# Kernel tuning notes

Hardware: AMD Instinct MI355X
Metric: run time of the kernel (lower is better)

## Reference

```python
import jax, jax.numpy as jnp
import numpy as np

D_MODEL = 512
D_STATE = 16
D_CONV = 4
EXPAND = 2
D_INNER = EXPAND * D_MODEL          # 1024
DT_RANK = D_MODEL // 16             # 32 (canonical 'auto' dt_rank)
EPS = 1e-5


def setup_inputs() -> dict:
    key = jax.random.key(0)
    ks = jax.random.split(key, 12)
    w = lambda i, shape, s=0.02: (jax.random.normal(ks[i], shape, jnp.float32) * s)
    inp = {
        "x": jax.random.normal(ks[0], (2, 1024, D_MODEL), jnp.float32),
        # pre-mixer LayerNorm
        "ln1_g": jnp.ones((D_MODEL,), jnp.float32),
        "ln1_b": jnp.zeros((D_MODEL,), jnp.float32),
        # Mamba SSM params
        "in_proj_w": w(1, (2 * D_INNER, D_MODEL)),
        "conv_w": w(2, (D_INNER, D_CONV), 0.1),
        "conv_b": jnp.zeros((D_INNER,), jnp.float32),
        "x_proj_w": w(3, (DT_RANK + 2 * D_STATE, D_INNER)),
        "dt_proj_w": w(4, (D_INNER, DT_RANK), 0.1),
        "dt_proj_b": w(5, (D_INNER,), 0.1),
        "A_log": jnp.log(jnp.broadcast_to(
            jnp.arange(1, D_STATE + 1, dtype=jnp.float32), (D_INNER, D_STATE))),
        "D": jnp.ones((D_INNER,), jnp.float32),
        "out_proj_w": w(6, (D_MODEL, D_INNER)),
        # FFN sub-block
        "ln2_g": jnp.ones((D_MODEL,), jnp.float32),
        "ln2_b": jnp.zeros((D_MODEL,), jnp.float32),
        "ffn1_w": w(7, (4 * D_MODEL, D_MODEL)),
        "ffn1_b": jnp.zeros((4 * D_MODEL,), jnp.float32),
        "ffn2_w": w(8, (D_MODEL, 4 * D_MODEL)),
        "ffn2_b": jnp.zeros((D_MODEL,), jnp.float32),
    }
    return inp


def _layernorm(x, g, b):
    mu = jnp.mean(x, axis=-1, keepdims=True)
    var = jnp.var(x, axis=-1, keepdims=True)
    return (x - mu) * jax.lax.rsqrt(var + EPS) * g + b


def _mamba(x, in_proj_w, conv_w, conv_b, x_proj_w, dt_proj_w, dt_proj_b,
           A_log, D, out_proj_w):
    B, L, _ = x.shape
    # input projection -> (x_in, gate z), each [B, L, E]
    xz = jnp.einsum('bld,ed->ble', x, in_proj_w)
    xi, z = jnp.split(xz, 2, axis=-1)
    # depthwise causal conv1d (width D_CONV): left-pad, cross-correlate
    xp = jnp.pad(xi, ((0, 0), (D_CONV - 1, 0), (0, 0)))
    xc = conv_b
    for k in range(D_CONV):
        xc = xc + xp[:, k:k + L, :] * conv_w[:, k]
    xc = jax.nn.silu(xc)  # [B, L, E]
    # data-dependent SSM parameters
    x_dbl = jnp.einsum('ble,re->blr', xc, x_proj_w)
    dt, Bc, Cc = jnp.split(x_dbl, [DT_RANK, DT_RANK + D_STATE], axis=-1)
    delta = jax.nn.softplus(jnp.einsum('blr,er->ble', dt, dt_proj_w) + dt_proj_b)
    A = -jnp.exp(A_log)  # [E, N]
    # discretize: deltaA, deltaBx both [B, L, E, N]
    deltaA = jnp.exp(delta[..., None] * A)
    deltaBx = delta[..., None] * Bc[:, :, None, :] * xc[..., None]

    def step(h, inputs):
        dA, dBx, C = inputs                       # [B,E,N],[B,E,N],[B,N]
        h = dA * h + dBx
        y = jnp.einsum('ben,bn->be', h, C)
        return h, y

    h0 = jnp.zeros((B, D_INNER, D_STATE), x.dtype)
    _, ys = jax.lax.scan(step, h0,
                         (jnp.swapaxes(deltaA, 0, 1),
                          jnp.swapaxes(deltaBx, 0, 1),
                          jnp.swapaxes(Cc, 0, 1)))
    y = jnp.swapaxes(ys, 0, 1) + xc * D           # [B, L, E]
    y = y * jax.nn.silu(z)
    return jnp.einsum('ble,de->bld', y, out_proj_w)


def reference(x, ln1_g, ln1_b, in_proj_w, conv_w, conv_b, x_proj_w,
              dt_proj_w, dt_proj_b, A_log, D, out_proj_w,
              ln2_g, ln2_b, ffn1_w, ffn1_b, ffn2_w, ffn2_b):
    # pre-norm Mamba mixer + residual (dropout = identity in eval mode)
    h = _mamba(_layernorm(x, ln1_g, ln1_b), in_proj_w, conv_w, conv_b,
               x_proj_w, dt_proj_w, dt_proj_b, A_log, D, out_proj_w)
    x = x + h
    # pre-norm FFN + residual
    f = _layernorm(x, ln2_g, ln2_b)
    f = jax.nn.gelu(jnp.einsum('bld,fd->blf', f, ffn1_w) + ffn1_b)
    f = jnp.einsum('blf,df->bld', f, ffn2_w) + ffn2_b
    return x + f
```

## Files before the change

kernel.cpp:

```cpp
#include <hip/hip_runtime.h>
#include <cmath>

typedef unsigned short u16;
typedef __attribute__((ext_vector_type(8))) short bf16x8;
typedef __attribute__((ext_vector_type(4))) float f32x4;

#define BB    2
#define LSEQ  1024
#define DM    512
#define DI    1024
#define NTOK  2048
#define NC    64
#define CL    16

__device__ __forceinline__ float siluf(float x) {
    return x * (1.0f / (1.0f + __expf(-x)));
}
__device__ __forceinline__ float geluf(float x) {
    float c = 0.7978845608028654f * (x + 0.044715f * x * x * x);
    return 0.5f * x * (1.0f + tanhf(c));
}
__device__ __forceinline__ u16 f2bf(float f) {
    union { float f; unsigned u; } v; v.f = f;
    unsigned r = v.u + 0x7fff + ((v.u >> 16) & 1);
    return (u16)(r >> 16);
}
__device__ __forceinline__ float bf2f(u16 u) {
    union { unsigned u; float f; } v; v.u = ((unsigned)u) << 16; return v.f;
}
__device__ __forceinline__ void async_cp16(const u16* g, u16* l) {
    __builtin_amdgcn_global_load_lds(
        (const __attribute__((address_space(1))) void*)g,
        (__attribute__((address_space(3))) void*)l, 16, 0, 0);
}

#define NCVT 3680

__global__ void prep_kernel(const float* __restrict__ s0, u16* __restrict__ d0,
                            const float* __restrict__ s1, u16* __restrict__ d1,
                            const float* __restrict__ s2, u16* __restrict__ d2,
                            const float* __restrict__ s3, u16* __restrict__ d3,
                            const float* __restrict__ s4, u16* __restrict__ d4,
                            const float* __restrict__ s5, u16* __restrict__ d5,
                            const float* __restrict__ x, const float* __restrict__ g,
                            const float* __restrict__ b, u16* __restrict__ lnb)
{
    __shared__ float shs[4], shq[4];
    __shared__ float smu, srs;
    if (blockIdx.x < NCVT) {
        int i = (blockIdx.x * 256 + threadIdx.x) * 4;
        const float* sp; u16* dp; int off;
        if      (i < 1048576) { sp = s0; dp = d0; off = i; }
        else if (i < 1572864) { sp = s1; dp = d1; off = i - 1048576; }
        else if (i < 2621440) { sp = s2; dp = d2; off = i - 1572864; }
        else if (i < 3670016) { sp = s3; dp = d3; off = i - 2621440; }
        else if (i < 3735552) { sp = s4; dp = d4; off = i - 3670016; }
        else                  { sp = s5; dp = d5; off = i - 3735552; }
        float4 v = *(const float4*)(sp + off);
        ushort4 o;
        o.x = f2bf(v.x); o.y = f2bf(v.y); o.z = f2bf(v.z); o.w = f2bf(v.w);
        *(ushort4*)(dp + off) = o;
        return;
    }
    int t = blockIdx.x - NCVT;
    int tid = threadIdx.x;
    const float* xr = x + (size_t)t * DM;
    float v0 = xr[tid];
    float v1 = xr[tid + 256];
    float rsum = v0 + v1;
    float rsq  = v0 * v0 + v1 * v1;
    #pragma unroll
    for (int o = 32; o > 0; o >>= 1) { rsum += __shfl_down(rsum, o); rsq += __shfl_down(rsq, o); }
    int wid = tid >> 6, lane = tid & 63;
    if (lane == 0) { shs[wid] = rsum; shq[wid] = rsq; }
    __syncthreads();
    if (tid == 0) {
        float a  = shs[0] + shs[1] + shs[2] + shs[3];
        float a2 = shq[0] + shq[1] + shq[2] + shq[3];
        float mu = a / DM;
        float var = a2 / DM - mu * mu;
        smu = mu;
        srs = rsqrtf(var + 1e-5f);
    }
    __syncthreads();
    float mu = smu, rs = srs;
    u16* orow = lnb + (size_t)t * DM;
    orow[tid]       = f2bf((v0 - mu) * rs * g[tid]       + b[tid]);
    orow[tid + 256] = f2bf((v1 - mu) * rs * g[tid + 256] + b[tid + 256]);
}

__global__ void ln_bf16_kernel(const float* __restrict__ x, const float* __restrict__ g,
                               const float* __restrict__ b, u16* __restrict__ out)
{
    int t = blockIdx.x;
    int tid = threadIdx.x;
    const float* xr = x + (size_t)t * DM;
    float v0 = xr[tid];
    float v1 = xr[tid + 256];
    float rsum = v0 + v1;
    float rsq  = v0 * v0 + v1 * v1;
    #pragma unroll
    for (int o = 32; o > 0; o >>= 1) { rsum += __shfl_down(rsum, o); rsq += __shfl_down(rsq, o); }
    __shared__ float shs[4], shq[4];
    __shared__ float smu, srs;
    int wid = tid >> 6, lane = tid & 63;
    if (lane == 0) { shs[wid] = rsum; shq[wid] = rsq; }
    __syncthreads();
    if (tid == 0) {
        float a  = shs[0] + shs[1] + shs[2] + shs[3];
        float a2 = shq[0] + shq[1] + shq[2] + shq[3];
        float mu = a / DM;
        float var = a2 / DM - mu * mu;
        smu = mu;
        srs = rsqrtf(var + 1e-5f);
    }
    __syncthreads();
    float mu = smu, rs = srs;
    u16* orow = out + (size_t)t * DM;
    orow[tid]       = f2bf((v0 - mu) * rs * g[tid]       + b[tid]);
    orow[tid + 256] = f2bf((v1 - mu) * rs * g[tid + 256] + b[tid + 256]);
}

template<int EPI, int BM, int BN, int BK, int OBF>
__global__ __launch_bounds__(256)
void mgemm_kernel(const u16* __restrict__ A, const u16* __restrict__ W, int K,
                  void* __restrict__ Cp, int ldc,
                  const float* __restrict__ bias, const float* __restrict__ resid, int ldr)
{
    __shared__ u16 As[BM * BK];
    __shared__ u16 Bs[BN * BK];
    constexpr int WR = BM / 2, WC = BN / 2;
    constexpr int MR = WR / 16, NR = WC / 16;
    constexpr int LPR = BK / 8;
    constexpr int CH_ROWS = 64 / LPR;
    constexpr int NCH_A = BM / CH_ROWS, NCH_B = BN / CH_ROWS;

    const int tid = threadIdx.x;
    const int wave = tid >> 6, lane = tid & 63;
    const int wm = wave >> 1, wn = wave & 1;
    const int m0 = blockIdx.y * BM, n0 = blockIdx.x * BN;
    const int crow = lane / LPR, ckoff = (lane % LPR) * 8;
    const int fr = lane & 15;

    f32x4 acc[MR][NR] = {};

    for (int k0 = 0; k0 < K; k0 += BK) {
        for (int c = wave; c < NCH_A; c += 4)
            async_cp16(A + (size_t)(m0 + c * CH_ROWS + crow) * K + k0 + ckoff, &As[c * 512]);
        for (int c = wave; c < NCH_B; c += 4)
            async_cp16(W + (size_t)(n0 + c * CH_ROWS + crow) * K + k0 + ckoff, &Bs[c * 512]);
        __syncthreads();
        #pragma unroll
        for (int ks = 0; ks < BK / 32; ++ks) {
            const int fk = ks * 32 + ((lane >> 4) << 3);
            bf16x8 af[MR], bv[NR];
            #pragma unroll
            for (int i = 0; i < MR; ++i)
                af[i] = *(const bf16x8*)&As[(wm * WR + i * 16 + fr) * BK + fk];
            #pragma unroll
            for (int j = 0; j < NR; ++j)
                bv[j] = *(const bf16x8*)&Bs[(wn * WC + j * 16 + fr) * BK + fk];
            #pragma unroll
            for (int i = 0; i < MR; ++i)
                #pragma unroll
                for (int j = 0; j < NR; ++j)
                    acc[i][j] = __builtin_amdgcn_mfma_f32_16x16x32_bf16(af[i], bv[j], acc[i][j], 0, 0, 0);
        }
        __syncthreads();
    }

    const int rbase = (lane >> 4) << 2;
    #pragma unroll
    for (int i = 0; i < MR; ++i) {
        #pragma unroll
        for (int j = 0; j < NR; ++j) {
            const int col  = n0 + wn * WC + j * 16 + fr;
            const int row0 = m0 + wm * WR + i * 16 + rbase;
            float bvv = (EPI == 4) ? bias[col] : 0.0f;
            #pragma unroll
            for (int r = 0; r < 4; ++r) {
                float v = acc[i][j][r];
                if (EPI == 3) v += resid[(size_t)(row0 + r) * ldr + col];
                if (EPI == 4) v += bvv + resid[(size_t)(row0 + r) * ldr + col];
                if (OBF) ((u16*)Cp)[(size_t)(row0 + r) * ldc + col] = f2bf(v);
                else     ((float*)Cp)[(size_t)(row0 + r) * ldc + col] = v;
            }
        }
    }
}

template<int EPI, int OBF>
__global__ __launch_bounds__(512)
void mgemm8_kernel(const u16* __restrict__ A, const u16* __restrict__ W, int K,
                   void* __restrict__ Cp, int ldc, const float* __restrict__ bias)
{
    constexpr int BM = 128, BN = 128, BK = 64;
    __shared__ u16 As[BM * BK];
    __shared__ u16 Bs[BN * BK];
    const int tid = threadIdx.x;
    const int wave = tid >> 6, lane = tid & 63;
    const int wm = wave >> 2, wn = wave & 3;
    const int m0 = blockIdx.y * BM, n0 = blockIdx.x * BN;
    const int crow = lane >> 3, ckoff = (lane & 7) * 8;
    const int fr = lane & 15;

    f32x4 acc[4][2] = {};

    for (int k0 = 0; k0 < K; k0 += BK) {
        #pragma unroll
        for (int c = wave; c < 16; c += 8)
            async_cp16(A + (size_t)(m0 + c * 8 + crow) * K + k0 + ckoff, &As[c * 512]);
        #pragma unroll
        for (int c = wave; c < 16; c += 8)
            async_cp16(W + (size_t)(n0 + c * 8 + crow) * K + k0 + ckoff, &Bs[c * 512]);
        __syncthreads();
        #pragma unroll
        for (int ks = 0; ks < 2; ++ks) {
            const int fk = ks * 32 + ((lane >> 4) << 3);
            bf16x8 af[4], bv[2];
            #pragma unroll
            for (int i = 0; i < 4; ++i)
                af[i] = *(const bf16x8*)&As[(wm * 64 + i * 16 + fr) * BK + fk];
            #pragma unroll
            for (int j = 0; j < 2; ++j)
                bv[j] = *(const bf16x8*)&Bs[(wn * 32 + j * 16 + fr) * BK + fk];
            #pragma unroll
            for (int i = 0; i < 4; ++i)
                #pragma unroll
                for (int j = 0; j < 2; ++j)
                    acc[i][j] = __builtin_amdgcn_mfma_f32_16x16x32_bf16(af[i], bv[j], acc[i][j], 0, 0, 0);
        }
        __syncthreads();
    }

    const int rbase = (lane >> 4) << 2;
    #pragma unroll
    for (int i = 0; i < 4; ++i) {
        #pragma unroll
        for (int j = 0; j < 2; ++j) {
            const int col  = n0 + wn * 32 + j * 16 + fr;
            const int row0 = m0 + wm * 64 + i * 16 + rbase;
            float bvv = (EPI == 2) ? bias[col] : 0.0f;
            #pragma unroll
            for (int r = 0; r < 4; ++r) {
                float v = acc[i][j][r];
                if (EPI == 2) v = geluf(v + bvv);
                if (OBF) ((u16*)Cp)[(size_t)(row0 + r) * ldc + col] = f2bf(v);
                else     ((float*)Cp)[(size_t)(row0 + r) * ldc + col] = v;
            }
        }
    }
}

__global__ __launch_bounds__(256)
void xproj_part_kernel(const u16* __restrict__ A, const u16* __restrict__ W,
                       float* __restrict__ P)
{
    constexpr int BM = 64, BK = 128;
    __shared__ u16 As[BM * BK];
    __shared__ u16 Bs[64 * BK];
    const int tid = threadIdx.x;
    const int wave = tid >> 6, lane = tid & 63;
    const int wm = wave >> 1, wn = wave & 1;
    const int ks = blockIdx.x;
    const int m0 = blockIdx.y * BM;
    const int k0 = ks * BK;
    const int crow = lane >> 4, ckoff = (lane & 15) * 8;
    const int fr = lane & 15;

    for (int c = wave; c < 16; c += 4) {
        async_cp16(A + (size_t)(m0 + c * 4 + crow) * 1024 + k0 + ckoff, &As[c * 512]);
        async_cp16(W + (size_t)(c * 4 + crow) * 1024 + k0 + ckoff, &Bs[c * 512]);
    }
    __syncthreads();

    f32x4 acc[2][2] = {};
    #pragma unroll
    for (int ks2 = 0; ks2 < 4; ++ks2) {
        const int fk = ks2 * 32 + ((lane >> 4) << 3);
        bf16x8 af[2], bv[2];
        #pragma unroll
        for (int i = 0; i < 2; ++i)
            af[i] = *(const bf16x8*)&As[(wm * 32 + i * 16 + fr) * BK + fk];
        #pragma unroll
        for (int j = 0; j < 2; ++j)
            bv[j] = *(const bf16x8*)&Bs[(wn * 32 + j * 16 + fr) * BK + fk];
        #pragma unroll
        for (int i = 0; i < 2; ++i)
            #pragma unroll
            for (int j = 0; j < 2; ++j)
                acc[i][j] = __builtin_amdgcn_mfma_f32_16x16x32_bf16(af[i], bv[j], acc[i][j], 0, 0, 0);
    }

    const int rbase = (lane >> 4) << 2;
    float* Pk = P + (size_t)ks * NTOK * 64;
    #pragma unroll
    for (int i = 0; i < 2; ++i)
        #pragma unroll
        for (int j = 0; j < 2; ++j) {
            const int col  = wn * 32 + j * 16 + fr;
            const int row0 = m0 + wm * 32 + i * 16 + rbase;
            #pragma unroll
            for (int r = 0; r < 4; ++r)
                Pk[(size_t)(row0 + r) * 64 + col] = acc[i][j][r];
        }
}

__global__ void xproj_reduce_kernel(const float* __restrict__ P, float* __restrict__ xdbl,
                                    u16* __restrict__ dtb)
{
    int i = blockIdx.x * 256 + threadIdx.x;
    float s = 0.0f;
    #pragma unroll
    for (int ks = 0; ks < 8; ++ks) s += P[(size_t)ks * NTOK * 64 + i];
    xdbl[i] = s;
    int col = i & 63;
    if (col < 32) dtb[(i >> 6) * 32 + col] = f2bf(s);
}

__global__ void conv_silu_kernel(const u16* __restrict__ xz,
                                 const float* __restrict__ cw,
                                 const float* __restrict__ cb,
                                 u16* __restrict__ xcb)
{
    int idx = blockIdx.x * 256 + threadIdx.x;
    int e8 = idx & (DI / 8 - 1);
    int e  = e8 * 8;
    int t  = idx >> 7;
    int l  = t & (LSEQ - 1);
    const u16* base = xz + (size_t)t * 2048 + e;
    bf16x8 r0 = {}, r1 = {}, r2 = {}, r3;
    r3 = *(const bf16x8*)(base);
    if (l >= 1) r2 = *(const bf16x8*)(base - 2048);
    if (l >= 2) r1 = *(const bf16x8*)(base - 2 * 2048);
    if (l >= 3) r0 = *(const bf16x8*)(base - 3 * 2048);
    float o[8];
    #pragma unroll
    for (int j = 0; j < 8; ++j) {
        const float4 w = *(const float4*)(cw + (e + j) * 4);
        float acc = cb[e + j];
        acc = fmaf(bf2f((u16)r0[j]), w.x, acc);
        acc = fmaf(bf2f((u16)r1[j]), w.y, acc);
        acc = fmaf(bf2f((u16)r2[j]), w.z, acc);
        acc = fmaf(bf2f((u16)r3[j]), w.w, acc);
        o[j] = siluf(acc);
    }
    bf16x8 obf;
    #pragma unroll
    for (int j = 0; j < 8; ++j) obf[j] = (short)f2bf(o[j]);
    *(bf16x8*)(xcb + (size_t)t * DI + e) = obf;
}

__device__ __forceinline__ float delta_of(const u16* __restrict__ dtb, size_t tok,
                                          const bf16x8* wv, float dbias)
{
    float dt = dbias;
    const u16* dr = dtb + tok * 32;
    #pragma unroll
    for (int q = 0; q < 4; ++q) {
        bf16x8 dv = *(const bf16x8*)(dr + q * 8);
        #pragma unroll
        for (int k = 0; k < 8; ++k)
            dt = fmaf(bf2f((u16)dv[k]), bf2f((u16)wv[q][k]), dt);
    }
    return (dt < 20.0f) ? log1pf(__expf(dt)) : dt;
}

__global__ void scanA_kernel(const u16* __restrict__ dtb,
                             const u16* __restrict__ wdt,
                             const float* __restrict__ dt_bias,
                             const u16* __restrict__ xcb,
                             const float* __restrict__ xdbl,
                             const float* __restrict__ A_log,
                             float* __restrict__ qbuf,
                             float* __restrict__ sumd)
{
    int i = blockIdx.x * 256 + threadIdx.x;
    int e = i & (DI - 1);
    int c = (i >> 10) & (NC - 1);
    int b = i >> 16;
    float Ae[16], h[16];
    #pragma unroll
    for (int n = 0; n < 16; ++n) { Ae[n] = -__expf(A_log[e * 16 + n]); h[n] = 0.0f; }
    const float dbias = dt_bias[e];
    bf16x8 wv[4];
    #pragma unroll
    for (int q = 0; q < 4; ++q) wv[q] = *(const bf16x8*)(wdt + e * 32 + q * 8);
    float sd = 0.0f;
    int l0 = c * CL;
    for (int l = 0; l < CL; ++l) {
        size_t tok = (size_t)b * LSEQ + l0 + l;
        float d = delta_of(dtb, tok, wv, dbias);
        float xcv = bf2f(xcb[tok * DI + e]);
        sd += d;
        float dx = d * xcv;
        const float4* B4 = (const float4*)(xdbl + tok * 64 + 32);
        #pragma unroll
        for (int q = 0; q < 4; ++q) {
            float4 Bq = B4[q];
            h[4*q+0] = __expf(d * Ae[4*q+0]) * h[4*q+0] + dx * Bq.x;
            h[4*q+1] = __expf(d * Ae[4*q+1]) * h[4*q+1] + dx * Bq.y;
            h[4*q+2] = __expf(d * Ae[4*q+2]) * h[4*q+2] + dx * Bq.z;
            h[4*q+3] = __expf(d * Ae[4*q+3]) * h[4*q+3] + dx * Bq.w;
        }
    }
    size_t base = ((size_t)(b * DI + e) * NC + c) * 16;
    #pragma unroll
    for (int n = 0; n < 16; ++n) qbuf[base + n] = h[n];
    sumd[(size_t)(b * DI + e) * NC + c] = sd;
}

__global__ void scanB_kernel(const float* __restrict__ qbuf,
                             const float* __restrict__ sumd,
                             const float* __restrict__ A_log,
                             float* __restrict__ hin)
{
    int i = blockIdx.x * 256 + threadIdx.x;
    int n = i & 15;
    int e = (i >> 4) & (DI - 1);
    int b = i >> 14;
    float Ae = -__expf(A_log[e * 16 + n]);
    float h = 0.0f;
    size_t base = (size_t)(b * DI + e) * NC;
    for (int c = 0; c < NC; ++c) {
        hin[(base + c) * 16 + n] = h;
        float P = __expf(Ae * sumd[base + c]);
        h = P * h + qbuf[(base + c) * 16 + n];
    }
}

__global__ void scanC_kernel(const u16* __restrict__ dtb,
                             const u16* __restrict__ wdt,
                             const float* __restrict__ dt_bias,
                             const u16* __restrict__ xcb,
                             const float* __restrict__ xdbl,
                             const u16* __restrict__ xz,
                             const float* __restrict__ A_log,
                             const float* __restrict__ Dp,
                             const float* __restrict__ hin,
                             u16* __restrict__ y)
{
    int i = blockIdx.x * 256 + threadIdx.x;
    int e = i & (DI - 1);
    int c = (i >> 10) & (NC - 1);
    int b = i >> 16;
    float Ae[16], h[16];
    size_t base = ((size_t)(b * DI + e) * NC + c) * 16;
    #pragma unroll
    for (int n = 0; n < 16; ++n) {
        Ae[n] = -__expf(A_log[e * 16 + n]);
        h[n] = hin[base + n];
    }
    const float dbias = dt_bias[e];
    bf16x8 wv[4];
    #pragma unroll
    for (int q = 0; q < 4; ++q) wv[q] = *(const bf16x8*)(wdt + e * 32 + q * 8);
    float Dv = Dp[e];
    int l0 = c * CL;
    for (int l = 0; l < CL; ++l) {
        size_t tok = (size_t)b * LSEQ + l0 + l;
        float d = delta_of(dtb, tok, wv, dbias);
        float xcv = bf2f(xcb[tok * DI + e]);
        float zv  = bf2f(xz[tok * 2048 + DI + e]);
        float dx = d * xcv;
        const float4* B4 = (const float4*)(xdbl + tok * 64 + 32);
        const float4* C4 = (const float4*)(xdbl + tok * 64 + 48);
        float yv = 0.0f;
        #pragma unroll
        for (int q = 0; q < 4; ++q) {
            float4 Bq = B4[q];
            float4 Cq = C4[q];
            float hb;
            hb = __expf(d * Ae[4*q+0]) * h[4*q+0] + dx * Bq.x; h[4*q+0] = hb; yv = fmaf(hb, Cq.x, yv);
            hb = __expf(d * Ae[4*q+1]) * h[4*q+1] + dx * Bq.y; h[4*q+1] = hb; yv = fmaf(hb, Cq.y, yv);
            hb = __expf(d * Ae[4*q+2]) * h[4*q+2] + dx * Bq.z; h[4*q+2] = hb; yv = fmaf(hb, Cq.z, yv);
            hb = __expf(d * Ae[4*q+3]) * h[4*q+3] + dx * Bq.w; h[4*q+3] = hb; yv = fmaf(hb, Cq.w, yv);
        }
        yv += xcv * Dv;
        yv *= siluf(zv);
        y[tok * DI + e] = f2bf(yv);
    }
}

extern "C" void kernel_launch(void* const* d_in, const int* in_sizes, int n_in,
                              void* d_out, int out_size, void* d_ws, size_t ws_size,
                              hipStream_t stream)
{
    const float* x         = (const float*)d_in[0];
    const float* ln1_g     = (const float*)d_in[1];
    const float* ln1_b     = (const float*)d_in[2];
    const float* in_proj_w = (const float*)d_in[3];
    const float* conv_w    = (const float*)d_in[4];
    const float* conv_b    = (const float*)d_in[5];
    const float* x_proj_w  = (const float*)d_in[6];
    const float* dt_proj_w = (const float*)d_in[7];
    const float* dt_proj_b = (const float*)d_in[8];
    const float* A_log     = (const float*)d_in[9];
    const float* Dp        = (const float*)d_in[10];
    const float* out_proj_w= (const float*)d_in[11];
    const float* ln2_g     = (const float*)d_in[12];
    const float* ln2_b     = (const float*)d_in[13];
    const float* ffn1_w    = (const float*)d_in[14];
    const float* ffn1_b    = (const float*)d_in[15];
    const float* ffn2_w    = (const float*)d_in[16];
    const float* ffn2_b    = (const float*)d_in[17];
    float* out = (float*)d_out;

    char* wsb = (char*)d_ws;
    u16*   lnb   = (u16*)wsb;    wsb += (size_t)2048 * 512 * 2;
    u16*   xzb   = (u16*)wsb;    wsb += (size_t)2048 * 2048 * 2;
    u16*   xcb   = (u16*)wsb;    wsb += (size_t)2048 * 1024 * 2;
    float* xdbl  = (float*)wsb;  wsb += (size_t)2048 * 64 * 4;
    u16*   dtb   = (u16*)wsb;    wsb += (size_t)2048 * 32 * 2;
    float* Ppart = (float*)wsb;  wsb += (size_t)8 * 2048 * 64 * 4;
    float* qbuf  = (float*)wsb;  wsb += (size_t)2048 * NC * 16 * 4;
    float* sumd  = (float*)wsb;  wsb += (size_t)BB * DI * NC * 4;
    float* hin   = (float*)wsb;  wsb += (size_t)2048 * NC * 16 * 4;
    u16*   ybuf  = (u16*)wsb;    wsb += (size_t)2048 * 1024 * 2;
    float* x2    = (float*)wsb;  wsb += (size_t)2048 * 512 * 4;
    u16*   ffnm  = (u16*)wsb;    wsb += (size_t)2048 * 2048 * 2;
    u16*   w_in  = (u16*)wsb;    wsb += (size_t)2048 * 512 * 2;
    u16*   w_out = (u16*)wsb;    wsb += (size_t)512 * 1024 * 2;
    u16*   w_f1  = (u16*)wsb;    wsb += (size_t)2048 * 512 * 2;
    u16*   w_f2  = (u16*)wsb;    wsb += (size_t)512 * 2048 * 2;
    u16*   w_x   = (u16*)wsb;    wsb += (size_t)64 * 1024 * 2;
    u16*   w_dt  = (u16*)wsb;    wsb += (size_t)1024 * 32 * 2;

    prep_kernel<<<NCVT + NTOK, 256, 0, stream>>>(in_proj_w, w_in, out_proj_w, w_out,
                                                 ffn1_w, w_f1, ffn2_w, w_f2,
                                                 x_proj_w, w_x, dt_proj_w, w_dt,
                                                 x, ln1_g, ln1_b, lnb);
    mgemm8_kernel<0,1><<<dim3(16,16), 512, 0, stream>>>(lnb, w_in, 512, xzb, 2048, nullptr);
    conv_silu_kernel<<<(NTOK * DI) / (256 * 8), 256, 0, stream>>>(xzb, conv_w, conv_b, xcb);
    xproj_part_kernel<<<dim3(8, 32), 256, 0, stream>>>(xcb, w_x, Ppart);
    xproj_reduce_kernel<<<(NTOK * 64) / 256, 256, 0, stream>>>(Ppart, xdbl, dtb);
    scanA_kernel<<<(BB * NC * DI) / 256, 256, 0, stream>>>(dtb, w_dt, dt_proj_b, xcb, xdbl, A_log, qbuf, sumd);
    scanB_kernel<<<(BB * DI * 16) / 256, 256, 0, stream>>>(qbuf, sumd, A_log, hin);
    scanC_kernel<<<(BB * NC * DI) / 256, 256, 0, stream>>>(dtb, w_dt, dt_proj_b, xcb, xdbl, xzb, A_log, Dp, hin, ybuf);
    mgemm_kernel<3,64,64,128,0><<<dim3(8,32), 256, 0, stream>>>(ybuf, w_out, 1024, x2, 512, nullptr, x, 512);
    ln_bf16_kernel<<<NTOK, 256, 0, stream>>>(x2, ln2_g, ln2_b, lnb);
    mgemm8_kernel<2,1><<<dim3(16,16), 512, 0, stream>>>(lnb, w_f1, 512, ffnm, 2048, ffn1_b);
    mgemm_kernel<4,64,64,128,0><<<dim3(8,32), 256, 0, stream>>>(ffnm, w_f2, 2048, out, 512, ffn2_b, x2, 512);
}
```

Baseline: 171.7 us.

## Transpose scan chunk-state buffers to e-contiguous bf16 and unify GEMM kernels

The chunked-scan intermediate buffers (qbuf, hin, sumd) move from an [b,e,c,n] layout to [b,c,n,e], so adjacent threads (consecutive e) write and read coalesced addresses. qbuf and hin are also stored as bf16, which halves their traffic. scanB is remapped so that threads index e fastest. The 512-thread mgemm8 kernel is removed, and the in_proj and ffn1 GEMMs now use the generic mgemm template with 128x64 tiles, with a GELU-bias epilogue added to it. Storing the chunk states in bf16 reduces the precision of the carried state.

```diff
diff --git a/kernel.cpp b/kernel.cpp
--- a/kernel.cpp
+++ b/kernel.cpp
@@ -176,75 +176,13 @@
         for (int j = 0; j < NR; ++j) {
             const int col  = n0 + wn * WC + j * 16 + fr;
             const int row0 = m0 + wm * WR + i * 16 + rbase;
-            float bvv = (EPI == 4) ? bias[col] : 0.0f;
-            #pragma unroll
-            for (int r = 0; r < 4; ++r) {
-                float v = acc[i][j][r];
-                if (EPI == 3) v += resid[(size_t)(row0 + r) * ldr + col];
-                if (EPI == 4) v += bvv + resid[(size_t)(row0 + r) * ldr + col];
-                if (OBF) ((u16*)Cp)[(size_t)(row0 + r) * ldc + col] = f2bf(v);
-                else     ((float*)Cp)[(size_t)(row0 + r) * ldc + col] = v;
-            }
-        }
-    }
-}
-
-template<int EPI, int OBF>
-__global__ __launch_bounds__(512)
-void mgemm8_kernel(const u16* __restrict__ A, const u16* __restrict__ W, int K,
-                   void* __restrict__ Cp, int ldc, const float* __restrict__ bias)
-{
-    constexpr int BM = 128, BN = 128, BK = 64;
-    __shared__ u16 As[BM * BK];
-    __shared__ u16 Bs[BN * BK];
-    const int tid = threadIdx.x;
-    const int wave = tid >> 6, lane = tid & 63;
-    const int wm = wave >> 2, wn = wave & 3;
-    const int m0 = blockIdx.y * BM, n0 = blockIdx.x * BN;
-    const int crow = lane >> 3, ckoff = (lane & 7) * 8;
-    const int fr = lane & 15;
-
-    f32x4 acc[4][2] = {};
-
-    for (int k0 = 0; k0 < K; k0 += BK) {
-        #pragma unroll
-        for (int c = wave; c < 16; c += 8)
-            async_cp16(A + (size_t)(m0 + c * 8 + crow) * K + k0 + ckoff, &As[c * 512]);
-        #pragma unroll
-        for (int c = wave; c < 16; c += 8)
-            async_cp16(W + (size_t)(n0 + c * 8 + crow) * K + k0 + ckoff, &Bs[c * 512]);
-        __syncthreads();
-        #pragma unroll
-        for (int ks = 0; ks < 2; ++ks) {
-            const int fk = ks * 32 + ((lane >> 4) << 3);
-            bf16x8 af[4], bv[2];
-            #pragma unroll
-            for (int i = 0; i < 4; ++i)
-                af[i] = *(const bf16x8*)&As[(wm * 64 + i * 16 + fr) * BK + fk];
-            #pragma unroll
-            for (int j = 0; j < 2; ++j)
-                bv[j] = *(const bf16x8*)&Bs[(wn * 32 + j * 16 + fr) * BK + fk];
-            #pragma unroll
-            for (int i = 0; i < 4; ++i)
-                #pragma unroll
-                for (int j = 0; j < 2; ++j)
-                    acc[i][j] = __builtin_amdgcn_mfma_f32_16x16x32_bf16(af[i], bv[j], acc[i][j], 0, 0, 0);
-        }
-        __syncthreads();
-    }
-
-    const int rbase = (lane >> 4) << 2;
-    #pragma unroll
-    for (int i = 0; i < 4; ++i) {
-        #pragma unroll
-        for (int j = 0; j < 2; ++j) {
-            const int col  = n0 + wn * 32 + j * 16 + fr;
-            const int row0 = m0 + wm * 64 + i * 16 + rbase;
-            float bvv = (EPI == 2) ? bias[col] : 0.0f;
+            float bvv = (EPI == 2 || EPI == 4) ? bias[col] : 0.0f;
             #pragma unroll
             for (int r = 0; r < 4; ++r) {
                 float v = acc[i][j][r];
                 if (EPI == 2) v = geluf(v + bvv);
+                if (EPI == 3) v += resid[(size_t)(row0 + r) * ldr + col];
+                if (EPI == 4) v += bvv + resid[(size_t)(row0 + r) * ldr + col];
                 if (OBF) ((u16*)Cp)[(size_t)(row0 + r) * ldc + col] = f2bf(v);
                 else     ((float*)Cp)[(size_t)(row0 + r) * ldc + col] = v;
             }
@@ -372,13 +310,14 @@
                              const u16* __restrict__ xcb,
                              const float* __restrict__ xdbl,
                              const float* __restrict__ A_log,
-                             float* __restrict__ qbuf,
+                             u16* __restrict__ qbuf,
                              float* __restrict__ sumd)
 {
     int i = blockIdx.x * 256 + threadIdx.x;
     int e = i & (DI - 1);
-    int c = (i >> 10) & (NC - 1);
-    int b = i >> 16;
+    int bc = i >> 10;
+    int c = bc & (NC - 1);
+    int b = bc >> 6;
     float Ae[16], h[16];
     #pragma unroll
     for (int n = 0; n < 16; ++n) { Ae[n] = -__expf(A_log[e * 16 + n]); h[n] = 0.0f; }
@@ -404,28 +343,29 @@
             h[4*q+3] = __expf(d * Ae[4*q+3]) * h[4*q+3] + dx * Bq.w;
         }
     }
-    size_t base = ((size_t)(b * DI + e) * NC + c) * 16;
-    #pragma unroll
-    for (int n = 0; n < 16; ++n) qbuf[base + n] = h[n];
-    sumd[(size_t)(b * DI + e) * NC + c] = sd;
-}
-
-__global__ void scanB_kernel(const float* __restrict__ qbuf,
+    size_t qbase = (size_t)bc * 16 * DI + e;
+    #pragma unroll
+    for (int n = 0; n < 16; ++n) qbuf[qbase + (size_t)n * DI] = f2bf(h[n]);
+    sumd[(size_t)bc * DI + e] = sd;
+}
+
+__global__ void scanB_kernel(const u16* __restrict__ qbuf,
                              const float* __restrict__ sumd,
                              const float* __restrict__ A_log,
-                             float* __restrict__ hin)
+                             u16* __restrict__ hin)
 {
     int i = blockIdx.x * 256 + threadIdx.x;
-    int n = i & 15;
-    int e = (i >> 4) & (DI - 1);
-    int b = i >> 14;
+    int e = i & (DI - 1);
+    int bn = i >> 10;
+    int n = bn & 15;
+    int b = bn >> 4;
     float Ae = -__expf(A_log[e * 16 + n]);
     float h = 0.0f;
-    size_t base = (size_t)(b * DI + e) * NC;
     for (int c = 0; c < NC; ++c) {
-        hin[(base + c) * 16 + n] = h;
-        float P = __expf(Ae * sumd[base + c]);
-        h = P * h + qbuf[(base + c) * 16 + n];
+        size_t idx = ((size_t)((b * NC + c) * 16 + n)) * DI + e;
+        hin[idx] = f2bf(h);
+        float P = __expf(Ae * sumd[(size_t)(b * NC + c) * DI + e]);
+        h = P * h + bf2f(qbuf[idx]);
     }
 }
 
@@ -437,19 +377,20 @@
                              const u16* __restrict__ xz,
                              const float* __restrict__ A_log,
                              const float* __restrict__ Dp,
-                             const float* __restrict__ hin,
+                             const u16* __restrict__ hin,
                              u16* __restrict__ y)
 {
     int i = blockIdx.x * 256 + threadIdx.x;
     int e = i & (DI - 1);
-    int c = (i >> 10) & (NC - 1);
-    int b = i >> 16;
+    int bc = i >> 10;
+    int c = bc & (NC - 1);
+    int b = bc >> 6;
     float Ae[16], h[16];
-    size_t base = ((size_t)(b * DI + e) * NC + c) * 16;
+    size_t hbase = (size_t)bc * 16 * DI + e;
     #pragma unroll
     for (int n = 0; n < 16; ++n) {
         Ae[n] = -__expf(A_log[e * 16 + n]);
-        h[n] = hin[base + n];
+        h[n] = bf2f(hin[hbase + (size_t)n * DI]);
     }
     const float dbias = dt_bias[e];
     bf16x8 wv[4];
@@ -513,9 +454,9 @@
     float* xdbl  = (float*)wsb;  wsb += (size_t)2048 * 64 * 4;
     u16*   dtb   = (u16*)wsb;    wsb += (size_t)2048 * 32 * 2;
     float* Ppart = (float*)wsb;  wsb += (size_t)8 * 2048 * 64 * 4;
-    float* qbuf  = (float*)wsb;  wsb += (size_t)2048 * NC * 16 * 4;
-    float* sumd  = (float*)wsb;  wsb += (size_t)BB * DI * NC * 4;
-    float* hin   = (float*)wsb;  wsb += (size_t)2048 * NC * 16 * 4;
+    u16*   qbuf  = (u16*)wsb;    wsb += (size_t)BB * NC * 16 * DI * 2;
+    float* sumd  = (float*)wsb;  wsb += (size_t)BB * NC * DI * 4;
+    u16*   hin   = (u16*)wsb;    wsb += (size_t)BB * NC * 16 * DI * 2;
     u16*   ybuf  = (u16*)wsb;    wsb += (size_t)2048 * 1024 * 2;
     float* x2    = (float*)wsb;  wsb += (size_t)2048 * 512 * 4;
     u16*   ffnm  = (u16*)wsb;    wsb += (size_t)2048 * 2048 * 2;
@@ -530,15 +471,15 @@
                                                  ffn1_w, w_f1, ffn2_w, w_f2,
                                                  x_proj_w, w_x, dt_proj_w, w_dt,
                                                  x, ln1_g, ln1_b, lnb);
-    mgemm8_kernel<0,1><<<dim3(16,16), 512, 0, stream>>>(lnb, w_in, 512, xzb, 2048, nullptr);
+    mgemm_kernel<0,128,64,64,1><<<dim3(32,16), 256, 0, stream>>>(lnb, w_in, 512, xzb, 2048, nullptr, nullptr, 0);
     conv_silu_kernel<<<(NTOK * DI) / (256 * 8), 256, 0, stream>>>(xzb, conv_w, conv_b, xcb);
     xproj_part_kernel<<<dim3(8, 32), 256, 0, stream>>>(xcb, w_x, Ppart);
     xproj_reduce_kernel<<<(NTOK * 64) / 256, 256, 0, stream>>>(Ppart, xdbl, dtb);
     scanA_kernel<<<(BB * NC * DI) / 256, 256, 0, stream>>>(dtb, w_dt, dt_proj_b, xcb, xdbl, A_log, qbuf, sumd);
-    scanB_kernel<<<(BB * DI * 16) / 256, 256, 0, stream>>>(qbuf, sumd, A_log, hin);
+    scanB_kernel<<<(BB * 16 * DI) / 256, 256, 0, stream>>>(qbuf, sumd, A_log, hin);
     scanC_kernel<<<(BB * NC * DI) / 256, 256, 0, stream>>>(dtb, w_dt, dt_proj_b, xcb, xdbl, xzb, A_log, Dp, hin, ybuf);
     mgemm_kernel<3,64,64,128,0><<<dim3(8,32), 256, 0, stream>>>(ybuf, w_out, 1024, x2, 512, nullptr, x, 512);
     ln_bf16_kernel<<<NTOK, 256, 0, stream>>>(x2, ln2_g, ln2_b, lnb);
-    mgemm8_kernel<2,1><<<dim3(16,16), 512, 0, stream>>>(lnb, w_f1, 512, ffnm, 2048, ffn1_b);
+    mgemm_kernel<2,128,64,64,1><<<dim3(32,16), 256, 0, stream>>>(lnb, w_f1, 512, ffnm, 2048, ffn1_b, nullptr, 0);
     mgemm_kernel<4,64,64,128,0><<<dim3(8,32), 256, 0, stream>>>(ffnm, w_f2, 2048, out, 512, ffn2_b, x2, 512);
 }
```

Result: no change. 171.2 us (-0.3%).
